# Optimization experiments

Hardware: AMD Instinct MI355X
Metric: run time of the kernel (lower is better)

The kernel has to match this reference:

```python
import jax, jax.numpy as jnp
import numpy as np

NUM_HEADS = 8
HEAD_SIZE = 64  # hidden_dim // num_heads = 512 // 8
SCALE = 1.0 / np.sqrt(HEAD_SIZE).astype(np.float32)
CAUSAL = True


def setup_inputs() -> dict:
    key = jax.random.key(0)
    k1, k2, k3 = jax.random.split(key, 3)
    b, s, d = 4, 2048, 512
    x = jax.random.normal(k1, (b, s, d), dtype=jnp.float32)
    w_qkv = jax.random.normal(k2, (d, 3 * d), dtype=jnp.float32) * 0.02
    b_qkv = jnp.zeros((3 * d,), dtype=jnp.float32)
    w_out = jax.random.normal(k3, (d, d), dtype=jnp.float32) * 0.02
    b_out = jnp.zeros((d,), dtype=jnp.float32)
    return {"x": x, "w_qkv": w_qkv, "b_qkv": b_qkv, "w_out": w_out, "b_out": b_out}


def reference(x, w_qkv, b_qkv, w_out, b_out):
    b, s, d = x.shape
    h, hd = NUM_HEADS, HEAD_SIZE
    qkv = x @ w_qkv + b_qkv                      # (b, s, 3d)
    q, k, v = jnp.split(qkv, 3, axis=-1)
    # (b, s, d) -> (b, h, s, hd)
    q = q.reshape(b, s, h, hd).transpose(0, 2, 1, 3)
    k = k.reshape(b, s, h, hd).transpose(0, 2, 1, 3)
    v = v.reshape(b, s, h, hd).transpose(0, 2, 1, 3)
    scores = jnp.einsum('bhqd,bhkd->bhqk', q, k) * SCALE  # (b, h, s, s)
    if CAUSAL:
        causal_mask = jnp.triu(jnp.ones((s, s), dtype=bool), k=1)
        scores = jnp.where(causal_mask, -jnp.inf, scores)
    attn = jax.nn.softmax(scores, axis=-1)
    out = jnp.einsum('bhqk,bhkd->bhqd', attn, v)          # (b, h, s, hd)
    out = out.transpose(0, 2, 1, 3).reshape(b, s, d)
    return out @ w_out + b_out
```

## Files before the change

### kernel.cpp

```cpp
#include <hip/hip_runtime.h>
#include <hip/hip_bf16.h>

#define BATCH 4
#define SEQ   2048
#define DM    512
#define NH    8
#define HD    64
#define PART  (BATCH*NH*SEQ*HD)
#define QSCALE 0.18033688f

typedef unsigned short u16;
typedef unsigned int   u32;
typedef __bf16 bf16x8 __attribute__((ext_vector_type(8)));
typedef float  f32x4  __attribute__((ext_vector_type(4)));
typedef float  f32x16 __attribute__((ext_vector_type(16)));
typedef unsigned int u32x2 __attribute__((ext_vector_type(2)));

__device__ __forceinline__ u16 f2bf(float f) {
    union { float f; u32 u; } v; v.f = f;
    u32 r = v.u + 0x7fffu + ((v.u >> 16) & 1u);
    return (u16)(r >> 16);
}

__device__ __forceinline__ void glds16(const u16* g, u16* lds) {
    __builtin_amdgcn_global_load_lds(
        (const __attribute__((address_space(1))) void*)g,
        (__attribute__((address_space(3))) void*)lds, 16, 0, 0);
}

__device__ __forceinline__ void pl32swap(u32 &a, u32 &b) {
    u32x2 r = __builtin_amdgcn_permlane32_swap(a, b, false, false);
    a = r[0]; b = r[1];
}

__global__ __launch_bounds__(256) void prep_k(
    const float* __restrict__ x, u16* __restrict__ xb,
    const float* __restrict__ w_qkv, u16* __restrict__ t_qkv,
    const float* __restrict__ w_out, u16* __restrict__ t_out)
{
    __shared__ u16 Ts[64][72];
    const int z = blockIdx.z, bx = blockIdx.x, t = threadIdx.x;

    if (z == 0) {
        const int n8 = PART / 8;
        for (int i = bx * 256 + t; i < n8; i += 512 * 256) {
            float4 a = *(const float4*)(x + (size_t)i * 8);
            float4 b = *(const float4*)(x + (size_t)i * 8 + 4);
            union { uint4 v; u16 s[8]; } o;
            o.s[0] = f2bf(a.x); o.s[1] = f2bf(a.y);
            o.s[2] = f2bf(a.z); o.s[3] = f2bf(a.w);
            o.s[4] = f2bf(b.x); o.s[5] = f2bf(b.y);
            o.s[6] = f2bf(b.z); o.s[7] = f2bf(b.w);
            *(uint4*)(xb + (size_t)i * 8) = o.v;
        }
        return;
    }
    const int N = (z == 1) ? 3 * DM : DM;
    const int ntiles = N / 64;
    if (bx >= ntiles * 8) return;
    const float* W = (z == 1) ? w_qkv : w_out;
    u16* Wt = (z == 1) ? t_qkv : t_out;
    const int n0 = (bx % ntiles) * 64, k0 = (bx / ntiles) * 64;

    #pragma unroll
    for (int l = 0; l < 4; ++l) {
        int idx = l * 1024 + t * 4;
        int r = idx >> 6, c = idx & 63;
        float4 v = *(const float4*)(W + (size_t)(k0 + r) * N + n0 + c);
        Ts[c + 0][r] = f2bf(v.x);
        Ts[c + 1][r] = f2bf(v.y);
        Ts[c + 2][r] = f2bf(v.z);
        Ts[c + 3][r] = f2bf(v.w);
    }
    __syncthreads();
    #pragma unroll
    for (int l = 0; l < 2; ++l) {
        int idx = l * 256 + t;
        int row = idx >> 3, ch = idx & 7;
        *(uint4*)(Wt + (size_t)(n0 + row) * DM + k0 + ch * 8) =
            *(const uint4*)(&Ts[row][ch * 8]);
    }
}

__global__ __launch_bounds__(512, 2) void gemm0_k(
    const u16* __restrict__ A, const u16* __restrict__ Bt,
    const float* __restrict__ bias, u16* __restrict__ ws)
{
    __shared__ __align__(16) u16 As[2][256 * 64];
    __shared__ __align__(16) u16 Bs[2][256 * 64];
    const int K = 512;

    const int tid = threadIdx.x, wave = tid >> 6, lane = tid & 63;
    const int l16 = lane & 15, quad = (lane >> 4) & 3;
    const int wm = wave >> 2, wn = wave & 3;
    const int bm0 = blockIdx.x * 256, bn0 = blockIdx.y * 256;

    const int srow8 = lane >> 3;
    const int lcx   = (lane & 7) ^ srow8;
    const u16* Agl = A  + (size_t)(bm0 + wave * 32 + srow8) * K + lcx * 8;
    const u16* Bgl = Bt + (size_t)(bn0 + wave * 32 + srow8) * K + lcx * 8;
    u16* adst = &As[0][wave * 2048];
    u16* bdst = &Bs[0][wave * 2048];

    int aoff[8][2], boff[4][2];
    #pragma unroll
    for (int mi = 0; mi < 8; ++mi)
        #pragma unroll
        for (int ks = 0; ks < 2; ++ks)
            aoff[mi][ks] = (wm * 128 + mi * 16 + l16) * 64 +
                           (((ks * 4 + quad)) ^ (l16 & 7)) * 8;
    #pragma unroll
    for (int ni = 0; ni < 4; ++ni)
        #pragma unroll
        for (int ks = 0; ks < 2; ++ks)
            boff[ni][ks] = (wn * 64 + ni * 16 + l16) * 64 +
                           (((ks * 4 + quad)) ^ (l16 & 7)) * 8;

    f32x4 acc[8][4];
    #pragma unroll
    for (int i = 0; i < 8; ++i)
        #pragma unroll
        for (int j = 0; j < 4; ++j)
            acc[i][j] = (f32x4){0.f, 0.f, 0.f, 0.f};

    #pragma unroll
    for (int i = 0; i < 4; ++i) {
        glds16(Agl + (size_t)i * 8 * K, adst + i * 512);
        glds16(Bgl + (size_t)i * 8 * K, bdst + i * 512);
    }
    __syncthreads();

    for (int it = 0; it < 8; ++it) {
        const int cur = it & 1;
        if (it < 7) {
            const int k0 = (it + 1) * 64;
            const int nxo = (cur ^ 1) * 16384;
            #pragma unroll
            for (int i = 0; i < 4; ++i) {
                glds16(Agl + k0 + (size_t)i * 8 * K, adst + nxo + i * 512);
                glds16(Bgl + k0 + (size_t)i * 8 * K, bdst + nxo + i * 512);
            }
        }
        const u16* Ab = &As[cur][0];
        const u16* Bb = &Bs[cur][0];
        #pragma unroll
        for (int ks = 0; ks < 2; ++ks) {
            bf16x8 bfr[4];
            #pragma unroll
            for (int ni = 0; ni < 4; ++ni)
                bfr[ni] = *(const bf16x8*)(&Bb[boff[ni][ks]]);
            __builtin_amdgcn_s_setprio(1);
            #pragma unroll
            for (int mi = 0; mi < 8; ++mi) {
                bf16x8 af = *(const bf16x8*)(&Ab[aoff[mi][ks]]);
                #pragma unroll
                for (int ni = 0; ni < 4; ++ni)
                    acc[mi][ni] = __builtin_amdgcn_mfma_f32_16x16x32_bf16(
                        af, bfr[ni], acc[mi][ni], 0, 0, 0);
            }
            __builtin_amdgcn_s_setprio(0);
        }
        __syncthreads();
    }

    #pragma unroll
    for (int mi = 0; mi < 8; ++mi) {
        #pragma unroll
        for (int ni = 0; ni < 4; ++ni) {
            int col = bn0 + wn * 64 + ni * 16 + l16;
            float bv = bias[col];
            int row0 = bm0 + wm * 128 + mi * 16 + quad * 4;
            float v[4];
            #pragma unroll
            for (int reg = 0; reg < 4; ++reg) v[reg] = acc[mi][ni][reg] + bv;

            int part = col >> 9, wi = col & 511;
            int h = wi >> 6, e = wi & 63;
            int b = row0 >> 11, s0 = row0 & 2047;
            if (part == 2) {
                union { u16 q[4]; uint2 u; } pk;
                #pragma unroll
                for (int reg = 0; reg < 4; ++reg) pk.q[reg] = f2bf(v[reg]);
                *(uint2*)(ws + (size_t)2 * PART +
                          ((size_t)(b * NH + h) * HD + e) * SEQ + s0) = pk.u;
            } else {
                float scl = (part == 0) ? QSCALE : 1.0f;
                #pragma unroll
                for (int reg = 0; reg < 4; ++reg)
                    ws[(size_t)part * PART +
                       ((size_t)(b * NH + h) * SEQ + s0 + reg) * HD + e] =
                        f2bf(v[reg] * scl);
            }
        }
    }
}

__global__ __launch_bounds__(256) void gemm1_k(
    const u16* __restrict__ A, const u16* __restrict__ Bt,
    const float* __restrict__ bias, float* __restrict__ out,
    int M, int N, int K)
{
    __shared__ __align__(16) u16 As[2][64 * 32];
    __shared__ __align__(16) u16 Bs[2][128 * 32];

    const int tid  = threadIdx.x;
    const int bm0  = blockIdx.x * 64;
    const int bn0  = blockIdx.y * 128;
    const int wave = tid >> 6, lane = tid & 63;
    const int l16  = lane & 15, quad = lane >> 4;
    const int wc   = wave * 32;

    const int srow = (lane >> 2);
    const int scol = (lane & 3) * 8;
    const int arow = wave * 16;
    const u16* Ag = A + (size_t)(bm0 + arow + srow) * K + scol;
    const u16* Bg = Bt + (size_t)(bn0 + wave * 32 + srow) * K + scol;
    const int wofsA = arow * 32;
    const int wofsB = (wave * 32) * 32;

    f32x4 acc[4][2];
    #pragma unroll
    for (int i = 0; i < 4; ++i)
        #pragma unroll
        for (int j = 0; j < 2; ++j)
            acc[i][j] = (f32x4){0.f, 0.f, 0.f, 0.f};

    glds16(Ag, &As[0][wofsA]);
    glds16(Bg,                  &Bs[0][wofsB]);
    glds16(Bg + (size_t)16 * K, &Bs[0][wofsB + 16 * 32]);
    __syncthreads();

    const int NIT = K >> 5;
    for (int it = 0; it < NIT; ++it) {
        const int cur = it & 1;
        if (it + 1 < NIT) {
            const int nx = cur ^ 1;
            const int k0 = (it + 1) << 5;
            glds16(Ag + k0, &As[nx][wofsA]);
            glds16(Bg + k0,                  &Bs[nx][wofsB]);
            glds16(Bg + k0 + (size_t)16 * K, &Bs[nx][wofsB + 16 * 32]);
        }

        bf16x8 af[4], bfr[2];
        #pragma unroll
        for (int mi = 0; mi < 4; ++mi)
            af[mi] = *(const bf16x8*)(&As[cur][(mi * 16 + l16) * 32 + quad * 8]);
        #pragma unroll
        for (int ni = 0; ni < 2; ++ni)
            bfr[ni] = *(const bf16x8*)(&Bs[cur][(wc + ni * 16 + l16) * 32 + quad * 8]);
        #pragma unroll
        for (int mi = 0; mi < 4; ++mi)
            #pragma unroll
            for (int ni = 0; ni < 2; ++ni)
                acc[mi][ni] = __builtin_amdgcn_mfma_f32_16x16x32_bf16(
                    af[mi], bfr[ni], acc[mi][ni], 0, 0, 0);
        __syncthreads();
    }

    #pragma unroll
    for (int mi = 0; mi < 4; ++mi) {
        #pragma unroll
        for (int ni = 0; ni < 2; ++ni) {
            int col = bn0 + wc + ni * 16 + l16;
            float bv = bias[col];
            int row0 = bm0 + mi * 16 + quad * 4;
            #pragma unroll
            for (int reg = 0; reg < 4; ++reg)
                out[(size_t)(row0 + reg) * N + col] = acc[mi][ni][reg] + bv;
        }
    }
}

__global__ __launch_bounds__(256, 4) void attn_k(
    const u16* __restrict__ Q, const u16* __restrict__ K,
    const u16* __restrict__ Vt, u16* __restrict__ O)
{
    __shared__ __align__(16) u16 KsB[2][64 * 64];
    __shared__ __align__(16) u16 VtB[2][64 * 64];
    __shared__ float Lred[4][32];

    const int bh = blockIdx.x;
    const int qt = 31 - blockIdx.y;
    const int tid = threadIdx.x, wave = tid >> 6, lane = tid & 63;
    const int l31 = lane & 31, hi = lane >> 5, x7 = lane & 7;
    const int qh = wave >> 1, kh = wave & 1;
    const size_t baseK = (size_t)bh * SEQ * HD;
    const size_t baseV = (size_t)bh * HD * SEQ;
    const int b = bh >> 3, h = bh & 7;

    const int sub = lane >> 3;
    const int lcx = (lane & 7) ^ sub;
    const u16* kg = K  + baseK + (size_t)((wave * 16 + sub) * 64)   + lcx * 8;
    const u16* vg = Vt + baseV + (size_t)((wave * 16 + sub) * 2048) + lcx * 8;
    u16* ksd = &KsB[0][wave * 1024];
    u16* vtd = &VtB[0][wave * 1024];

    int koff[4], voff[2][2];
    #pragma unroll
    for (int k = 0; k < 4; ++k)
        koff[k] = (kh * 32 + l31) * 64 + ((((k << 1) + hi)) ^ x7) * 8;
    #pragma unroll
    for (int dt = 0; dt < 2; ++dt)
        #pragma unroll
        for (int k0 = 0; k0 < 2; ++k0)
            voff[dt][k0] = (dt * 32 + l31) * 64 + ((kh * 4 + k0 * 2 + hi) ^ x7) * 8;

    const u16* qg = Q + baseK + (size_t)(qt * 64 + qh * 32 + l31) * 64 + hi * 8;
    bf16x8 qf[4];
    #pragma unroll
    for (int k = 0; k < 4; ++k)
        qf[k] = *(const bf16x8*)(qg + k * 16);

    glds16(kg,            ksd);
    glds16(kg + 8 * 64,   ksd + 512);
    glds16(vg,            vtd);
    glds16(vg + 8 * 2048, vtd + 512);
    __syncthreads();

    float la0 = 0.f, la1 = 0.f;
    f32x16 o0, o1;
    #pragma unroll
    for (int i = 0; i < 16; ++i) { o0[i] = 0.f; o1[i] = 0.f; }

    for (int kt = 0; kt <= qt; ++kt) {
        const int cur = kt & 1;
        if (kt < qt) {
            const int nx = (cur ^ 1) * 4096;
            glds16(kg + (size_t)(kt + 1) * 4096,          ksd + nx);
            glds16(kg + (size_t)(kt + 1) * 4096 + 8 * 64, ksd + nx + 512);
            glds16(vg + (size_t)(kt + 1) * 64,            vtd + nx);
            glds16(vg + (size_t)(kt + 1) * 64 + 8 * 2048, vtd + nx + 512);
        }

        const bool diag = (kt == qt);
        if (!(diag && kh > qh)) {
            bf16x8 kf[4], vf[2][2];
            #pragma unroll
            for (int k = 0; k < 4; ++k)
                kf[k] = *(const bf16x8*)(&KsB[cur][koff[k]]);
            #pragma unroll
            for (int dt = 0; dt < 2; ++dt)
                #pragma unroll
                for (int k0 = 0; k0 < 2; ++k0)
                    vf[dt][k0] = *(const bf16x8*)(&VtB[cur][voff[dt][k0]]);

            f32x16 st;
            #pragma unroll
            for (int i = 0; i < 16; ++i) st[i] = 0.f;
            __builtin_amdgcn_s_setprio(1);
            #pragma unroll
            for (int k = 0; k < 4; ++k)
                st = __builtin_amdgcn_mfma_f32_32x32x16_bf16(
                    kf[k], qf[k], st, 0, 0, 0);
            __builtin_amdgcn_s_setprio(0);

            float p[16];
            #pragma unroll
            for (int r = 0; r < 16; ++r)
                p[r] = __builtin_amdgcn_exp2f(st[r]);
            if (diag && kh == qh) {
                #pragma unroll
                for (int r = 0; r < 16; ++r) {
                    int kvl = (r & 3) + 8 * (r >> 2) + 4 * hi;
                    if (kvl > l31) p[r] = 0.f;
                }
            }
            #pragma unroll
            for (int r = 0; r < 8; ++r) { la0 += p[r]; la1 += p[r + 8]; }

            u32 c[8];
            #pragma unroll
            for (int m = 0; m < 8; ++m) {
                __hip_bfloat162 t =
                    __float22bfloat162_rn(float2{p[2 * m], p[2 * m + 1]});
                c[m] = *(u32*)&t;
            }
            pl32swap(c[0], c[2]); pl32swap(c[1], c[3]);
            pl32swap(c[4], c[6]); pl32swap(c[5], c[7]);
            union { u32 w[4]; bf16x8 v; } pa0, pa1;
            pa0.w[0] = c[0]; pa0.w[1] = c[1]; pa0.w[2] = c[2]; pa0.w[3] = c[3];
            pa1.w[0] = c[4]; pa1.w[1] = c[5]; pa1.w[2] = c[6]; pa1.w[3] = c[7];

            __builtin_amdgcn_s_setprio(1);
            o0 = __builtin_amdgcn_mfma_f32_32x32x16_bf16(pa0.v, vf[0][0], o0, 0, 0, 0);
            o0 = __builtin_amdgcn_mfma_f32_32x32x16_bf16(pa1.v, vf[0][1], o0, 0, 0, 0);
            o1 = __builtin_amdgcn_mfma_f32_32x32x16_bf16(pa0.v, vf[1][0], o1, 0, 0, 0);
            o1 = __builtin_amdgcn_mfma_f32_32x32x16_bf16(pa1.v, vf[1][1], o1, 0, 0, 0);
            __builtin_amdgcn_s_setprio(0);
        }
        __syncthreads();
    }

    float l2 = (la0 + la1);
    l2 += __shfl_xor(l2, 32);
    if (lane < 32) Lred[wave][lane] = l2;
    float* Ob = (qh == 0) ? (float*)&KsB[0][0] : (float*)&VtB[0][0];
    if (kh == 1) {
        #pragma unroll
        for (int r = 0; r < 16; ++r) {
            Ob[r * 64 + lane]        = o0[r];
            Ob[(16 + r) * 64 + lane] = o1[r];
        }
    }
    __syncthreads();
    if (kh == 0) {
        #pragma unroll
        for (int r = 0; r < 16; ++r) {
            int ql = (r & 3) + 8 * (r >> 2) + 4 * hi;
            float lt = Lred[2 * qh][ql] + Lred[2 * qh + 1][ql];
            int srow = qt * 64 + qh * 32 + ql;
            size_t idx = (((size_t)(b * SEQ + srow)) * NH + h) * HD + l31;
            float v0 = (o0[r] + Ob[r * 64 + lane]) / lt;
            float v1 = (o1[r] + Ob[(16 + r) * 64 + lane]) / lt;
            O[idx]      = f2bf(v0);
            O[idx + 32] = f2bf(v1);
        }
    }
}

extern "C" void kernel_launch(void* const* d_in, const int* in_sizes, int n_in,
                              void* d_out, int out_size, void* d_ws, size_t ws_size,
                              hipStream_t stream) {
    const float* x     = (const float*)d_in[0];
    const float* w_qkv = (const float*)d_in[1];
    const float* b_qkv = (const float*)d_in[2];
    const float* w_out = (const float*)d_in[3];
    const float* b_out = (const float*)d_in[4];

    u16* qkv    = (u16*)d_ws;
    u16* attn   = qkv + (size_t)3 * PART;
    u16* xb     = attn + (size_t)PART;
    u16* wt_qkv = xb + (size_t)PART;
    u16* wt_out = wt_qkv + (size_t)(3 * DM) * DM;

    const int M = BATCH * SEQ;

    prep_k<<<dim3(512, 1, 3), 256, 0, stream>>>(x, xb, w_qkv, wt_qkv,
                                                w_out, wt_out);

    dim3 g1(M / 256, (3 * DM) / 256);
    gemm0_k<<<g1, 512, 0, stream>>>(xb, wt_qkv, b_qkv, qkv);

    dim3 g2(BATCH * NH, 32);
    attn_k<<<g2, 256, 0, stream>>>(qkv, qkv + PART, qkv + 2 * (size_t)PART, attn);

    dim3 g3(M / 64, DM / 128);
    gemm1_k<<<g3, 256, 0, stream>>>(attn, wt_out, b_out, (float*)d_out, M, DM, DM);
}
```

Baseline: 151.1 us.

## Shrink QKV GEMM M-tile to 128 and prefetch two stages ahead with vmcnt waits

The QKV projection GEMM tile is cut from 256x256 to 128x256, which doubles the grid to 384 blocks and spreads the work across more CUs. The loop now keeps two k-tiles of loads in flight, waits on them with explicit s_waitcnt vmcnt counts plus raw barriers instead of __syncthreads, and issues the load for tile it+2 after compute. The aim is to hide global-to-LDS latency better and improve CU occupancy balance, at the cost of less reuse of B per block. Launch bounds drop to one block per SM hint, and correctness depends on the hand-coded vmcnt counts matching the six loads issued per stage.

Measured after the change: 153.1 us. No clear change (+1.3%).

```diff
diff --git a/kernel.cpp b/kernel.cpp
--- a/kernel.cpp
+++ b/kernel.cpp
@@ -82,94 +82,106 @@
     }
 }
 
-__global__ __launch_bounds__(512, 2) void gemm0_k(
+__global__ __launch_bounds__(512, 1) void gemm0_k(
     const u16* __restrict__ A, const u16* __restrict__ Bt,
     const float* __restrict__ bias, u16* __restrict__ ws)
 {
-    __shared__ __align__(16) u16 As[2][256 * 64];
+    __shared__ __align__(16) u16 As[2][128 * 64];
     __shared__ __align__(16) u16 Bs[2][256 * 64];
     const int K = 512;
 
     const int tid = threadIdx.x, wave = tid >> 6, lane = tid & 63;
     const int l16 = lane & 15, quad = (lane >> 4) & 3;
     const int wm = wave >> 2, wn = wave & 3;
-    const int bm0 = blockIdx.x * 256, bn0 = blockIdx.y * 256;
-
-    const int srow8 = lane >> 3;
-    const int lcx   = (lane & 7) ^ srow8;
-    const u16* Agl = A  + (size_t)(bm0 + wave * 32 + srow8) * K + lcx * 8;
-    const u16* Bgl = Bt + (size_t)(bn0 + wave * 32 + srow8) * K + lcx * 8;
-    u16* adst = &As[0][wave * 2048];
+    const int bm0 = blockIdx.x * 128, bn0 = blockIdx.y * 256;
+
+    const int sub8 = lane >> 3;
+    const int lcx  = (lane & 7) ^ sub8;
+    const u16* Agl = A  + (size_t)(bm0 + wave * 16 + sub8) * K + lcx * 8;
+    const u16* Bgl = Bt + (size_t)(bn0 + wave * 32 + sub8) * K + lcx * 8;
+    u16* adst = &As[0][wave * 1024];
     u16* bdst = &Bs[0][wave * 2048];
 
-    int aoff[8][2], boff[4][2];
-    #pragma unroll
-    for (int mi = 0; mi < 8; ++mi)
+    int aoff[4][2], boff[4][2];
+    #pragma unroll
+    for (int mi = 0; mi < 4; ++mi)
         #pragma unroll
         for (int ks = 0; ks < 2; ++ks)
-            aoff[mi][ks] = (wm * 128 + mi * 16 + l16) * 64 +
-                           (((ks * 4 + quad)) ^ (l16 & 7)) * 8;
+            aoff[mi][ks] = (wm * 64 + mi * 16 + l16) * 64 +
+                           ((ks * 4 + quad) ^ (l16 & 7)) * 8;
     #pragma unroll
     for (int ni = 0; ni < 4; ++ni)
         #pragma unroll
         for (int ks = 0; ks < 2; ++ks)
             boff[ni][ks] = (wn * 64 + ni * 16 + l16) * 64 +
-                           (((ks * 4 + quad)) ^ (l16 & 7)) * 8;
-
-    f32x4 acc[8][4];
-    #pragma unroll
-    for (int i = 0; i < 8; ++i)
+                           ((ks * 4 + quad) ^ (l16 & 7)) * 8;
+
+    f32x4 acc[4][4];
+    #pragma unroll
+    for (int i = 0; i < 4; ++i)
         #pragma unroll
         for (int j = 0; j < 4; ++j)
             acc[i][j] = (f32x4){0.f, 0.f, 0.f, 0.f};
 
     #pragma unroll
-    for (int i = 0; i < 4; ++i) {
-        glds16(Agl + (size_t)i * 8 * K, adst + i * 512);
-        glds16(Bgl + (size_t)i * 8 * K, bdst + i * 512);
-    }
-    __syncthreads();
+    for (int t = 0; t < 2; ++t) {
+        const int k0 = t * 64;
+        const int bo = t * 8192, bo2 = t * 16384;
+        glds16(Agl + k0,                   adst + bo);
+        glds16(Agl + k0 + (size_t)8 * K,   adst + bo + 512);
+        glds16(Bgl + k0,                   bdst + bo2);
+        glds16(Bgl + k0 + (size_t)8 * K,   bdst + bo2 + 512);
+        glds16(Bgl + k0 + (size_t)16 * K,  bdst + bo2 + 1024);
+        glds16(Bgl + k0 + (size_t)24 * K,  bdst + bo2 + 1536);
+    }
 
     for (int it = 0; it < 8; ++it) {
         const int cur = it & 1;
-        if (it < 7) {
-            const int k0 = (it + 1) * 64;
-            const int nxo = (cur ^ 1) * 16384;
-            #pragma unroll
-            for (int i = 0; i < 4; ++i) {
-                glds16(Agl + k0 + (size_t)i * 8 * K, adst + nxo + i * 512);
-                glds16(Bgl + k0 + (size_t)i * 8 * K, bdst + nxo + i * 512);
-            }
-        }
+        if (it < 7) asm volatile("s_waitcnt vmcnt(6)" ::: "memory");
+        else        asm volatile("s_waitcnt vmcnt(0)" ::: "memory");
+        __builtin_amdgcn_s_barrier();
+
         const u16* Ab = &As[cur][0];
         const u16* Bb = &Bs[cur][0];
         #pragma unroll
         for (int ks = 0; ks < 2; ++ks) {
-            bf16x8 bfr[4];
+            bf16x8 bfr[4], af[4];
             #pragma unroll
             for (int ni = 0; ni < 4; ++ni)
                 bfr[ni] = *(const bf16x8*)(&Bb[boff[ni][ks]]);
+            #pragma unroll
+            for (int mi = 0; mi < 4; ++mi)
+                af[mi] = *(const bf16x8*)(&Ab[aoff[mi][ks]]);
             __builtin_amdgcn_s_setprio(1);
             #pragma unroll
-            for (int mi = 0; mi < 8; ++mi) {
-                bf16x8 af = *(const bf16x8*)(&Ab[aoff[mi][ks]]);
+            for (int mi = 0; mi < 4; ++mi)
                 #pragma unroll
                 for (int ni = 0; ni < 4; ++ni)
                     acc[mi][ni] = __builtin_amdgcn_mfma_f32_16x16x32_bf16(
-                        af, bfr[ni], acc[mi][ni], 0, 0, 0);
-            }
+                        af[mi], bfr[ni], acc[mi][ni], 0, 0, 0);
             __builtin_amdgcn_s_setprio(0);
         }
-        __syncthreads();
-    }
-
-    #pragma unroll
-    for (int mi = 0; mi < 8; ++mi) {
+
+        __builtin_amdgcn_s_barrier();
+        if (it + 2 < 8) {
+            const int k0 = (it + 2) * 64;
+            const int bo = cur * 8192, bo2 = cur * 16384;
+            glds16(Agl + k0,                   adst + bo);
+            glds16(Agl + k0 + (size_t)8 * K,   adst + bo + 512);
+            glds16(Bgl + k0,                   bdst + bo2);
+            glds16(Bgl + k0 + (size_t)8 * K,   bdst + bo2 + 512);
+            glds16(Bgl + k0 + (size_t)16 * K,  bdst + bo2 + 1024);
+            glds16(Bgl + k0 + (size_t)24 * K,  bdst + bo2 + 1536);
+        }
+    }
+
+    #pragma unroll
+    for (int mi = 0; mi < 4; ++mi) {
         #pragma unroll
         for (int ni = 0; ni < 4; ++ni) {
             int col = bn0 + wn * 64 + ni * 16 + l16;
             float bv = bias[col];
-            int row0 = bm0 + wm * 128 + mi * 16 + quad * 4;
+            int row0 = bm0 + wm * 64 + mi * 16 + quad * 4;
             float v[4];
             #pragma unroll
             for (int reg = 0; reg < 4; ++reg) v[reg] = acc[mi][ni][reg] + bv;
@@ -438,7 +450,7 @@
     prep_k<<<dim3(512, 1, 3), 256, 0, stream>>>(x, xb, w_qkv, wt_qkv,
                                                 w_out, wt_out);
 
-    dim3 g1(M / 256, (3 * DM) / 256);
+    dim3 g1(M / 128, (3 * DM) / 256);
     gemm0_k<<<g1, 512, 0, stream>>>(xb, wt_qkv, b_qkv, qkv);
 
     dim3 g2(BATCH * NH, 32);
```
